# Kernel tuning notes

Measured on AMD Instinct MI355X. Metric: run time of the kernel, lower is better.

## Reference

```python
import math
import jax, jax.numpy as jnp
import numpy as np

D_MODEL = 1024
NUM_HEADS = 16
D_K = D_MODEL // NUM_HEADS
THETA = 10000.0
MAX_SEQ_LEN = 2048
BATCH = 2
SEQ = 2048


def build_rope_matrices(theta, d_k, max_seq_len):
    # Faithful to the torch buffer: per-position d_k x d_k tridiagonal rotation matrix.
    k = jnp.arange(d_k)
    inv_freq = jnp.power(theta, -2.0 * (k // 2) / d_k)  # [d_k]
    pos = jnp.arange(max_seq_len, dtype=jnp.float32)[:, None]  # [S,1]
    ang = pos * inv_freq[None, :]  # [S, d_k]
    cos_v = jnp.cos(ang)  # main diagonal
    sin_v = jnp.sin(jnp.where(k % 2 == 0, ang, 0.0))[:, :-1]  # sub/super diagonal, len d_k-1

    def mk(c, s):
        return jnp.diag(c) + jnp.diag(s, -1) + jnp.diag(-s, 1)

    return jax.vmap(mk)(cos_v, sin_v)  # [max_seq_len, d_k, d_k]


def setup_inputs() -> dict:
    key = jax.random.key(0)
    k1, k2, k3 = jax.random.split(key, 3)
    x = jax.random.normal(k1, (BATCH, SEQ, D_MODEL), dtype=jnp.float32)
    token_positions = jnp.arange(SEQ, dtype=jnp.int64 if jax.config.jax_enable_x64 else jnp.int32)
    # trunc_normal init approximated by scaled normal (same distribution family / scale)
    std_attn = 2.0 / (D_MODEL + 3 * D_MODEL)
    std_out = 2.0 / (D_MODEL + D_MODEL)
    W_attn = jax.random.normal(k2, (3 * NUM_HEADS * D_K, D_MODEL), dtype=jnp.float32) * std_attn
    W_out = jax.random.normal(k3, (D_MODEL, NUM_HEADS * D_K), dtype=jnp.float32) * std_out
    rope = build_rope_matrices(THETA, D_K, MAX_SEQ_LEN)
    return {"x": x, "W_attn": W_attn, "W_out": W_out, "rope": rope,
            "token_positions": token_positions}


def reference(x, W_attn, W_out, rope, token_positions):
    B, S, _ = x.shape
    # QKV projection: '... d_in, d_out d_in -> ... d_out'
    proj = jnp.einsum('bsd,ed->bse', x, W_attn)  # [B,S,3*H*dk]
    proj = proj.reshape(B, S, 3, NUM_HEADS, D_K)
    proj = jnp.transpose(proj, (2, 0, 3, 1, 4))  # [3,B,H,S,dk]
    Q, K, V = proj[0], proj[1], proj[2]
    # RoPE via per-position matrix multiply (faithful to module)
    R = rope[token_positions]  # [S, dk, dk]
    Q = jnp.einsum('sij,bhsj->bhsi', R, Q)
    K = jnp.einsum('sij,bhsj->bhsi', R, K)
    # naive causal attention with full score matrix (faithful)
    scores = jnp.einsum('bhnd,bhmd->bhnm', Q, K) / math.sqrt(D_K)
    causal = jnp.tril(jnp.ones((S, S), dtype=bool))
    scores = jnp.where(causal, scores, -jnp.inf)
    attn = jax.nn.softmax(scores, axis=-1)
    attended = jnp.einsum('bhnm,bhmd->bhnd', attn, V)  # [B,H,S,dk]
    concat = jnp.transpose(attended, (0, 2, 1, 3)).reshape(B, S, NUM_HEADS * D_K)
    return jnp.einsum('bse,de->bsd', concat, W_out)
```

## Files before the change

### kernel.cpp

```cpp
#include <hip/hip_runtime.h>
#include <math.h>

#define B_SZ 2
#define SEQ 2048
#define DMODEL 1024
#define NH 16
#define DK 64
#define NQKV 3072
#define M_ROWS 4096

#define NEG_BIG (-3.0e38f)
#define SCL 0.18033688011112042f

typedef short short8 __attribute__((ext_vector_type(8)));
typedef float v4f __attribute__((ext_vector_type(4)));
typedef unsigned short ushort_t;

__device__ inline ushort_t f2bf(float f) {
    unsigned u = __float_as_uint(f);
    u += 0x7fffu + ((u >> 16) & 1u);
    return (ushort_t)(u >> 16);
}

__device__ __forceinline__ unsigned cvt_pk_bf16(float lo, float hi) {
    unsigned r;
    asm("v_cvt_pk_bf16_f32 %0, %1, %2" : "=v"(r) : "v"(lo), "v"(hi));
    return r;
}
__device__ __forceinline__ void permlane32_swap(unsigned &a, unsigned &b) {
    asm("v_permlane32_swap_b32 %0, %1" : "+v"(a), "+v"(b));
}
__device__ __forceinline__ void permlane16_swap(unsigned &a, unsigned &b) {
    asm("v_permlane16_swap_b32 %0, %1" : "+v"(a), "+v"(b));
}

__device__ __forceinline__ void gl_lds16(const ushort_t* g, ushort_t* l) {
    __builtin_amdgcn_global_load_lds(
        (const __attribute__((address_space(1))) unsigned int*)g,
        (__attribute__((address_space(3))) unsigned int*)l, 16, 0, 0);
}

__global__ __launch_bounds__(256) void prep_kernel(
    const float* __restrict__ x, const float* __restrict__ Wa,
    const float* __restrict__ Wo, const float* __restrict__ rope,
    ushort_t* __restrict__ xb, ushort_t* __restrict__ Wab, ushort_t* __restrict__ Wob,
    float* __restrict__ cosT, float* __restrict__ sinT)
{
    const int bid = blockIdx.x;
    if (bid < 8192) {
        const float* src; ushort_t* dst; int i;
        if (bid < 4096)      { src = x;  dst = xb;  i = bid * 256 + threadIdx.x; }
        else if (bid < 7168) { src = Wa; dst = Wab; i = (bid - 4096) * 256 + threadIdx.x; }
        else                 { src = Wo; dst = Wob; i = (bid - 7168) * 256 + threadIdx.x; }
        float4 v = reinterpret_cast<const float4*>(src)[i];
        ushort4 r;
        r.x = f2bf(v.x); r.y = f2bf(v.y); r.z = f2bf(v.z); r.w = f2bf(v.w);
        reinterpret_cast<ushort4*>(dst)[i] = r;
    } else {
        const int i = (bid - 8192) * 256 + threadIdx.x;
        const int p = i >> 6, d = i & 63;
        const float* Rp = rope + (size_t)p * 4096;
        const float c = Rp[d * 64 + d];
        const float s = Rp[(d | 1) * 64 + (d & ~1)];
        cosT[i] = c;
        sinT[i] = (d & 1) ? s : -s;
    }
}

#define ES_STRIDE 136
extern __shared__ ushort_t qkv_smem[];

__global__ __launch_bounds__(256) void qkv_mfma_kernel(
    const ushort_t* __restrict__ xb,
    const ushort_t* __restrict__ Wab,
    const float* __restrict__ cosT, const float* __restrict__ sinT,
    const int* __restrict__ tpos,
    ushort_t* __restrict__ Qb, ushort_t* __restrict__ Kb, ushort_t* __restrict__ Vtb)
{
    ushort_t* Es = qkv_smem;

    const int tid = threadIdx.x;
    const int w = tid >> 6, lane = tid & 63;
    const int lm = lane & 15, g = lane >> 4;
    const int wm = (w >> 1) * 64, wn = (w & 1) * 64;
    const int e0 = blockIdx.x * 128, m0 = blockIdx.y * 128;

    int srow[8], skc[8];
#pragma unroll
    for (int j = 0; j < 8; ++j) {
        const int c = tid + 256 * j;
        const int cm = c & 1023;
        const int row = cm >> 3, pp = cm & 7;
        srow[j] = row;
        skc[j] = (pp ^ (row & 7)) * 8;
    }

    v4f acc[4][4] = {};

    for (int k0 = 0; k0 < DMODEL; k0 += 64) {
        __syncthreads();
#pragma unroll
        for (int j = 0; j < 4; ++j)
            gl_lds16(&Wab[(size_t)(e0 + srow[j]) * DMODEL + k0 + skc[j]],
                     &qkv_smem[(tid + 256 * j) * 8]);
#pragma unroll
        for (int j = 4; j < 8; ++j)
            gl_lds16(&xb [(size_t)(m0 + srow[j]) * DMODEL + k0 + skc[j]],
                     &qkv_smem[(tid + 256 * j) * 8]);
        __syncthreads();

#pragma unroll
        for (int kb = 0; kb < 2; ++kb) {
            short8 af[4], bfr[4];
#pragma unroll
            for (int mf = 0; mf < 4; ++mf) {
                const int r = wm + mf * 16 + lm;
                af[mf] = *reinterpret_cast<const short8*>(
                    &qkv_smem[(r * 8 + ((kb * 4 + g) ^ (r & 7))) * 8]);
            }
#pragma unroll
            for (int nf = 0; nf < 4; ++nf) {
                const int r = wn + nf * 16 + lm;
                bfr[nf] = *reinterpret_cast<const short8*>(
                    &qkv_smem[8192 + (r * 8 + ((kb * 4 + g) ^ (r & 7))) * 8]);
            }
#pragma unroll
            for (int mf = 0; mf < 4; ++mf)
#pragma unroll
                for (int nf = 0; nf < 4; ++nf)
                    acc[mf][nf] = __builtin_amdgcn_mfma_f32_16x16x32_bf16(af[mf], bfr[nf], acc[mf][nf], 0, 0, 0);
        }
    }

    __syncthreads();

    const int which = e0 >> 10;
    const int h0 = (e0 & 1023) >> 6;
    const int bb = m0 >> 11, s0 = m0 & 2047;

    if (which < 2) {
        ushort_t* buf = (which == 0) ? Qb : Kb;
        const float qs = (which == 0) ? SCL : 1.0f;
#pragma unroll
        for (int mf = 0; mf < 4; ++mf) {
            const int ebase = wm + mf * 16 + g * 4;
            const int d0 = (e0 + ebase) & 63;
#pragma unroll
            for (int nf = 0; nf < 4; ++nf) {
                const int sloc = wn + nf * 16 + lm;
                float v[4] = {acc[mf][nf][0], acc[mf][nf][1], acc[mf][nf][2], acc[mf][nf][3]};
                const int p = tpos[s0 + sloc];
                const float4 c4 = *reinterpret_cast<const float4*>(&cosT[p * 64 + d0]);
                const float4 s4 = *reinterpret_cast<const float4*>(&sinT[p * 64 + d0]);
                const float r0 = (c4.x * v[0] + s4.x * v[1]) * qs;
                const float r1 = (c4.y * v[1] + s4.y * v[0]) * qs;
                const float r2 = (c4.z * v[2] + s4.z * v[3]) * qs;
                const float r3 = (c4.w * v[3] + s4.w * v[2]) * qs;
                uint2 pp;
                pp.x = (unsigned)f2bf(r0) | ((unsigned)f2bf(r1) << 16);
                pp.y = (unsigned)f2bf(r2) | ((unsigned)f2bf(r3) << 16);
                *reinterpret_cast<uint2*>(&Es[sloc * ES_STRIDE + ebase]) = pp;
            }
        }
        __syncthreads();
#pragma unroll
        for (int hh = 0; hh < 2; ++hh) {
            ushort_t* dst = buf + (((size_t)bb * NH + h0 + hh) * SEQ + s0) * DK;
#pragma unroll
            for (int t = 0; t < 4; ++t) {
                const int o = (t * 256 + tid) * 8;
                const int sloc = o >> 6, d = o & 63;
                const short8 vv = *reinterpret_cast<const short8*>(&Es[sloc * ES_STRIDE + hh * 64 + d]);
                *reinterpret_cast<short8*>(&dst[o]) = vv;
            }
        }
    } else {
#pragma unroll
        for (int mf = 0; mf < 4; ++mf) {
            const int ebase = wm + mf * 16 + g * 4;
#pragma unroll
            for (int nf = 0; nf < 4; ++nf) {
                const int sloc = wn + nf * 16 + lm;
                Es[(ebase + 0) * ES_STRIDE + sloc] = f2bf(acc[mf][nf][0]);
                Es[(ebase + 1) * ES_STRIDE + sloc] = f2bf(acc[mf][nf][1]);
                Es[(ebase + 2) * ES_STRIDE + sloc] = f2bf(acc[mf][nf][2]);
                Es[(ebase + 3) * ES_STRIDE + sloc] = f2bf(acc[mf][nf][3]);
            }
        }
        __syncthreads();
#pragma unroll
        for (int t = 0; t < 8; ++t) {
            const int c = t * 256 + tid;
            const int hh = c >> 10, cm = c & 1023;
            const int d = cm >> 4, s8c = (cm & 15) * 8;
            const short8 vv = *reinterpret_cast<const short8*>(&Es[(hh * 64 + d) * ES_STRIDE + s8c]);
            ushort_t* dst = Vtb + ((size_t)bb * NH + h0 + hh) * SEQ * DK + (size_t)d * SEQ + s0 + s8c;
            *reinterpret_cast<short8*>(dst) = vv;
        }
    }
}

#define ATTN_STEP(QF0, QF1, QROW, LACC, OACC, DIAG, C0)                           \
    {                                                                             \
        v4f sacc[4] = {};                                                         \
        _Pragma("unroll")                                                         \
        for (int nf = 0; nf < 4; ++nf) {                                          \
            sacc[nf] = __builtin_amdgcn_mfma_f32_16x16x32_bf16(kf[nf][0], QF0, sacc[nf], 0, 0, 0); \
            sacc[nf] = __builtin_amdgcn_mfma_f32_16x16x32_bf16(kf[nf][1], QF1, sacc[nf], 0, 0, 0); \
        }                                                                         \
        if (DIAG) {                                                               \
            _Pragma("unroll")                                                     \
            for (int nf = 0; nf < 4; ++nf)                                        \
                _Pragma("unroll")                                                 \
                for (int reg = 0; reg < 4; ++reg) {                               \
                    const int kv = (C0) + nf * 16 + g * 4 + reg;                  \
                    if (kv > (QROW)) sacc[nf][reg] = NEG_BIG;                     \
                }                                                                 \
        }                                                                         \
        unsigned pk0[8];                                                          \
        _Pragma("unroll")                                                         \
        for (int nf = 0; nf < 4; ++nf) {                                          \
            pk0[nf * 2]     = cvt_pk_bf16(exp2f(sacc[nf][0]), exp2f(sacc[nf][1])); \
            pk0[nf * 2 + 1] = cvt_pk_bf16(exp2f(sacc[nf][2]), exp2f(sacc[nf][3])); \
        }                                                                         \
        _Pragma("unroll")                                                         \
        for (int kc = 0; kc < 2; ++kc) {                                          \
            unsigned x0 = pk0[kc * 4 + 0], y0 = pk0[kc * 4 + 2];                  \
            unsigned x1 = pk0[kc * 4 + 1], y1 = pk0[kc * 4 + 3];                  \
            permlane32_swap(x0, y0); permlane16_swap(x0, y0);                     \
            permlane32_swap(x1, y1); permlane16_swap(x1, y1);                     \
            union { unsigned u[4]; short8 s; } pu;                                \
            pu.u[0] = x0; pu.u[1] = x1; pu.u[2] = y0; pu.u[3] = y1;               \
            const short8 pf = pu.s;                                               \
            LACC = __builtin_amdgcn_mfma_f32_16x16x32_bf16(ones8, pf, LACC, 0, 0, 0); \
            _Pragma("unroll")                                                     \
            for (int df = 0; df < 4; ++df)                                        \
                OACC[df] = __builtin_amdgcn_mfma_f32_16x16x32_bf16(vf[df][kc], pf, OACC[df], 0, 0, 0); \
        }                                                                         \
    }

__global__ __launch_bounds__(256, 2) void attn_mfma_kernel(
    const ushort_t* __restrict__ Qb, const ushort_t* __restrict__ Kb,
    const ushort_t* __restrict__ Vtb, ushort_t* __restrict__ attb)
{
    __shared__ ushort_t Ks[2][64][72];
    __shared__ ushort_t Vs[2][64][72];

    const int tid = threadIdx.x;
    const int w = tid >> 6, lane = tid & 63;
    const int lm = lane & 15, g = lane >> 4, lk8 = g * 8;

    const int u = blockIdx.x;
    const int h = blockIdx.y, b = blockIdx.z;
    const size_t ho = ((size_t)b * NH + h) * SEQ * DK;
    const ushort_t* Qh = Qb + ho;
    const ushort_t* Kh = Kb + ho;
    const ushort_t* Vth = Vtb + ho;

    const int rr0 = tid >> 3, cc80 = (tid & 7) * 8;
    const int rr1 = (tid + 256) >> 3, cc81 = ((tid + 256) & 7) * 8;

    const int it1 = u, it2 = 31 - u;
    const int qrowA = it1 * 64 + w * 16 + lm;
    const int qrowB = it2 * 64 + w * 16 + lm;

    const short8 qa0 = *reinterpret_cast<const short8*>(&Qh[(size_t)qrowA * DK + lk8]);
    const short8 qa1 = *reinterpret_cast<const short8*>(&Qh[(size_t)qrowA * DK + 32 + lk8]);
    const short8 qb0 = *reinterpret_cast<const short8*>(&Qh[(size_t)qrowB * DK + lk8]);
    const short8 qb1 = *reinterpret_cast<const short8*>(&Qh[(size_t)qrowB * DK + 32 + lk8]);

    const short8 ones8 = {16256, 16256, 16256, 16256, 16256, 16256, 16256, 16256};

    v4f laccA = {}, laccB = {};
    v4f OA[4] = {}, OB[4] = {};

    short8 kreg[2], vreg[2];
    kreg[0] = *reinterpret_cast<const short8*>(&Kh[(size_t)rr0 * DK + cc80]);
    kreg[1] = *reinterpret_cast<const short8*>(&Kh[(size_t)rr1 * DK + cc81]);
    vreg[0] = *reinterpret_cast<const short8*>(&Vth[(size_t)rr0 * SEQ + cc80]);
    vreg[1] = *reinterpret_cast<const short8*>(&Vth[(size_t)rr1 * SEQ + cc81]);

    for (int jt = 0; jt <= it2; ++jt) {
        const int c0 = jt * 64;
        const int bufi = jt & 1;
        ushort_t (*Ksb)[72] = Ks[bufi];
        ushort_t (*Vsb)[72] = Vs[bufi];

        *reinterpret_cast<short8*>(&Ksb[rr0][cc80]) = kreg[0];
        *reinterpret_cast<short8*>(&Ksb[rr1][cc81]) = kreg[1];
        *reinterpret_cast<short8*>(&Vsb[rr0][cc80]) = vreg[0];
        *reinterpret_cast<short8*>(&Vsb[rr1][cc81]) = vreg[1];

        if (jt < it2) {
            const int c0n = c0 + 64;
            kreg[0] = *reinterpret_cast<const short8*>(&Kh[(size_t)(c0n + rr0) * DK + cc80]);
            kreg[1] = *reinterpret_cast<const short8*>(&Kh[(size_t)(c0n + rr1) * DK + cc81]);
            vreg[0] = *reinterpret_cast<const short8*>(&Vth[(size_t)rr0 * SEQ + c0n + cc80]);
            vreg[1] = *reinterpret_cast<const short8*>(&Vth[(size_t)rr1 * SEQ + c0n + cc81]);
        }

        __syncthreads();

        short8 kf[4][2], vf[4][2];
#pragma unroll
        for (int nf = 0; nf < 4; ++nf) {
            kf[nf][0] = *reinterpret_cast<const short8*>(&Ksb[nf * 16 + lm][lk8]);
            kf[nf][1] = *reinterpret_cast<const short8*>(&Ksb[nf * 16 + lm][32 + lk8]);
        }
#pragma unroll
        for (int df = 0; df < 4; ++df) {
            vf[df][0] = *reinterpret_cast<const short8*>(&Vsb[df * 16 + lm][lk8]);
            vf[df][1] = *reinterpret_cast<const short8*>(&Vsb[df * 16 + lm][32 + lk8]);
        }

        ATTN_STEP(qb0, qb1, qrowB, laccB, OB, (jt == it2), c0)
        if (jt <= it1) {
            ATTN_STEP(qa0, qa1, qrowA, laccA, OA, (jt == it1), c0)
        }
    }

    {
        const float inv = 1.0f / laccA[0];
#pragma unroll
        for (int df = 0; df < 4; ++df) {
            uint2 st;
            st.x = cvt_pk_bf16(OA[df][0] * inv, OA[df][1] * inv);
            st.y = cvt_pk_bf16(OA[df][2] * inv, OA[df][3] * inv);
            *reinterpret_cast<uint2*>(
                &attb[((size_t)b * SEQ + qrowA) * DMODEL + h * DK + df * 16 + g * 4]) = st;
        }
    }
    {
        const float inv = 1.0f / laccB[0];
#pragma unroll
        for (int df = 0; df < 4; ++df) {
            uint2 st;
            st.x = cvt_pk_bf16(OB[df][0] * inv, OB[df][1] * inv);
            st.y = cvt_pk_bf16(OB[df][2] * inv, OB[df][3] * inv);
            *reinterpret_cast<uint2*>(
                &attb[((size_t)b * SEQ + qrowB) * DMODEL + h * DK + df * 16 + g * 4]) = st;
        }
    }
}

__global__ __launch_bounds__(256) void out_mfma_kernel(
    const ushort_t* __restrict__ attb,
    const ushort_t* __restrict__ Wob,
    float* __restrict__ out)
{
    __shared__ ushort_t smem[16384];

    const int tid = threadIdx.x;
    const int w = tid >> 6, lane = tid & 63;
    const int lm = lane & 15, g = lane >> 4;
    const int wm = (w >> 1) * 64, wn = (w & 1) * 64;
    const int m0 = blockIdx.y * 128, n0 = blockIdx.x * 128;

    int srow[8], skc[8];
#pragma unroll
    for (int j = 0; j < 8; ++j) {
        const int c = tid + 256 * j;
        const int cm = c & 1023;
        const int row = cm >> 3, pp = cm & 7;
        srow[j] = row;
        skc[j] = (pp ^ (row & 7)) * 8;
    }

    v4f acc[4][4] = {};

    for (int k0 = 0; k0 < DMODEL; k0 += 64) {
        __syncthreads();
#pragma unroll
        for (int j = 0; j < 4; ++j)
            gl_lds16(&attb[(size_t)(m0 + srow[j]) * DMODEL + k0 + skc[j]],
                     &smem[(tid + 256 * j) * 8]);
#pragma unroll
        for (int j = 4; j < 8; ++j)
            gl_lds16(&Wob[(size_t)(n0 + srow[j]) * DMODEL + k0 + skc[j]],
                     &smem[(tid + 256 * j) * 8]);
        __syncthreads();

#pragma unroll
        for (int kb = 0; kb < 2; ++kb) {
            short8 af[4], bfr[4];
#pragma unroll
            for (int mf = 0; mf < 4; ++mf) {
                const int r = wm + mf * 16 + lm;
                af[mf] = *reinterpret_cast<const short8*>(
                    &smem[(r * 8 + ((kb * 4 + g) ^ (r & 7))) * 8]);
            }
#pragma unroll
            for (int nf = 0; nf < 4; ++nf) {
                const int r = wn + nf * 16 + lm;
                bfr[nf] = *reinterpret_cast<const short8*>(
                    &smem[8192 + (r * 8 + ((kb * 4 + g) ^ (r & 7))) * 8]);
            }
#pragma unroll
            for (int mf = 0; mf < 4; ++mf)
#pragma unroll
                for (int nf = 0; nf < 4; ++nf)
                    acc[mf][nf] = __builtin_amdgcn_mfma_f32_16x16x32_bf16(af[mf], bfr[nf], acc[mf][nf], 0, 0, 0);
        }
    }

#pragma unroll
    for (int mf = 0; mf < 4; ++mf)
#pragma unroll
        for (int reg = 0; reg < 4; ++reg) {
            const int m = m0 + wm + mf * 16 + g * 4 + reg;
#pragma unroll
            for (int nf = 0; nf < 4; ++nf) {
                const int n = n0 + wn + nf * 16 + lm;
                out[(size_t)m * DMODEL + n] = acc[mf][nf][reg];
            }
        }
}

extern "C" void kernel_launch(void* const* d_in, const int* in_sizes, int n_in,
                              void* d_out, int out_size, void* d_ws, size_t ws_size,
                              hipStream_t stream) {
    (void)in_sizes; (void)n_in; (void)out_size; (void)ws_size;

    const float* x    = (const float*)d_in[0];
    const float* Wa   = (const float*)d_in[1];
    const float* Wo   = (const float*)d_in[2];
    const float* rope = (const float*)d_in[3];
    const int*   tp   = (const int*)d_in[4];
    float* out = (float*)d_out;

    char* ws = (char*)d_ws;
    ushort_t* xb   = (ushort_t*)(ws);
    ushort_t* Wab  = (ushort_t*)(ws + (8u << 20));
    ushort_t* Wob  = (ushort_t*)(ws + (14u << 20));
    float*    cosT = (float*)   (ws + (16u << 20));
    float*    sinT = (float*)   (ws + (16u << 20) + (512u << 10));
    ushort_t* Qb   = (ushort_t*)(ws + (17u << 20));
    ushort_t* Kb   = (ushort_t*)(ws + (25u << 20));
    ushort_t* Vtb  = (ushort_t*)(ws + (33u << 20));
    ushort_t* attb = (ushort_t*)(ws + (41u << 20));

    dim3 blk(256);
    prep_kernel<<<dim3(8704), blk, 0, stream>>>(x, Wa, Wo, rope, xb, Wab, Wob, cosT, sinT);

    const size_t qkv_lds = 128 * ES_STRIDE * sizeof(ushort_t);
    qkv_mfma_kernel<<<dim3(NQKV / 128, M_ROWS / 128), blk, qkv_lds, stream>>>(
        xb, Wab, cosT, sinT, tp, Qb, Kb, Vtb);
    attn_mfma_kernel<<<dim3(16, NH, B_SZ), blk, 0, stream>>>(Qb, Kb, Vtb, attb);
    out_mfma_kernel<<<dim3(DMODEL / 128, M_ROWS / 128), blk, 0, stream>>>(attb, Wob, out);
}
```

Baseline: 217.4 us.

## Double-buffer LDS tiles and swizzle block order in QKV and output GEMMs

Both projection GEMMs now use two LDS buffers so the next K-tile's global-to-LDS loads are issued before computing the current tile, with explicit vmcnt waits and barriers replacing the two syncthreads per iteration. Block indices are remapped with an XCD-style swizzle so neighbouring tiles share L2, and MFMA sections get raised wave priority. The cost is double the LDS (64KB per block), which may reduce occupancy, and hand-placed waitcnt that depends on the exact count of outstanding loads.

```diff
diff --git a/kernel.cpp b/kernel.cpp
--- a/kernel.cpp
+++ b/kernel.cpp
@@ -68,7 +68,16 @@
 }
 
 #define ES_STRIDE 136
-extern __shared__ ushort_t qkv_smem[];
+
+#define QKV_STAGE(bofs, k0s)                                                   \
+    _Pragma("unroll")                                                          \
+    for (int j = 0; j < 4; ++j)                                                \
+        gl_lds16(&Wab[(size_t)(e0 + srow[j]) * DMODEL + (k0s) + skc[j]],       \
+                 &qkv_smem[(bofs) + (tid + 256 * j) * 8]);                     \
+    _Pragma("unroll")                                                          \
+    for (int j = 4; j < 8; ++j)                                                \
+        gl_lds16(&xb[(size_t)(m0 + srow[j]) * DMODEL + (k0s) + skc[j]],        \
+                 &qkv_smem[(bofs) + (tid + 256 * j) * 8]);
 
 __global__ __launch_bounds__(256) void qkv_mfma_kernel(
     const ushort_t* __restrict__ xb,
@@ -77,13 +86,17 @@
     const int* __restrict__ tpos,
     ushort_t* __restrict__ Qb, ushort_t* __restrict__ Kb, ushort_t* __restrict__ Vtb)
 {
+    __shared__ ushort_t qkv_smem[32768];
     ushort_t* Es = qkv_smem;
 
     const int tid = threadIdx.x;
     const int w = tid >> 6, lane = tid & 63;
     const int lm = lane & 15, g = lane >> 4;
     const int wm = (w >> 1) * 64, wn = (w & 1) * 64;
-    const int e0 = blockIdx.x * 128, m0 = blockIdx.y * 128;
+
+    const int lid = blockIdx.y * 24 + blockIdx.x;
+    const int swz = (lid & 7) * 96 + (lid >> 3);
+    const int e0 = (swz % 24) * 128, m0 = (swz / 24) * 128;
 
     int srow[8], skc[8];
 #pragma unroll
@@ -97,18 +110,23 @@
 
     v4f acc[4][4] = {};
 
-    for (int k0 = 0; k0 < DMODEL; k0 += 64) {
-        __syncthreads();
-#pragma unroll
-        for (int j = 0; j < 4; ++j)
-            gl_lds16(&Wab[(size_t)(e0 + srow[j]) * DMODEL + k0 + skc[j]],
-                     &qkv_smem[(tid + 256 * j) * 8]);
-#pragma unroll
-        for (int j = 4; j < 8; ++j)
-            gl_lds16(&xb [(size_t)(m0 + srow[j]) * DMODEL + k0 + skc[j]],
-                     &qkv_smem[(tid + 256 * j) * 8]);
-        __syncthreads();
-
+    QKV_STAGE(0, 0);
+
+    for (int t = 0; t < 16; ++t) {
+        const int bofs = (t & 1) << 14;
+        if (t < 15) {
+            const int nofs = ((t + 1) & 1) << 14;
+            QKV_STAGE(nofs, (t + 1) * 64);
+            __builtin_amdgcn_sched_barrier(0);
+            asm volatile("s_waitcnt vmcnt(8)" ::: "memory");
+        } else {
+            __builtin_amdgcn_sched_barrier(0);
+            asm volatile("s_waitcnt vmcnt(0)" ::: "memory");
+        }
+        __builtin_amdgcn_s_barrier();
+        __builtin_amdgcn_sched_barrier(0);
+
+        __builtin_amdgcn_s_setprio(1);
 #pragma unroll
         for (int kb = 0; kb < 2; ++kb) {
             short8 af[4], bfr[4];
@@ -116,13 +134,13 @@
             for (int mf = 0; mf < 4; ++mf) {
                 const int r = wm + mf * 16 + lm;
                 af[mf] = *reinterpret_cast<const short8*>(
-                    &qkv_smem[(r * 8 + ((kb * 4 + g) ^ (r & 7))) * 8]);
+                    &qkv_smem[bofs + (r * 8 + ((kb * 4 + g) ^ (r & 7))) * 8]);
             }
 #pragma unroll
             for (int nf = 0; nf < 4; ++nf) {
                 const int r = wn + nf * 16 + lm;
                 bfr[nf] = *reinterpret_cast<const short8*>(
-                    &qkv_smem[8192 + (r * 8 + ((kb * 4 + g) ^ (r & 7))) * 8]);
+                    &qkv_smem[bofs + 8192 + (r * 8 + ((kb * 4 + g) ^ (r & 7))) * 8]);
             }
 #pragma unroll
             for (int mf = 0; mf < 4; ++mf)
@@ -130,6 +148,11 @@
                 for (int nf = 0; nf < 4; ++nf)
                     acc[mf][nf] = __builtin_amdgcn_mfma_f32_16x16x32_bf16(af[mf], bfr[nf], acc[mf][nf], 0, 0, 0);
         }
+        __builtin_amdgcn_s_setprio(0);
+
+        __builtin_amdgcn_sched_barrier(0);
+        __builtin_amdgcn_s_barrier();
+        __builtin_amdgcn_sched_barrier(0);
     }
 
     __syncthreads();
@@ -343,18 +366,31 @@
     }
 }
 
+#define OUT_STAGE(bofs, k0s)                                                   \
+    _Pragma("unroll")                                                          \
+    for (int j = 0; j < 4; ++j)                                                \
+        gl_lds16(&attb[(size_t)(m0 + srow[j]) * DMODEL + (k0s) + skc[j]],      \
+                 &smem[(bofs) + (tid + 256 * j) * 8]);                         \
+    _Pragma("unroll")                                                          \
+    for (int j = 4; j < 8; ++j)                                                \
+        gl_lds16(&Wob[(size_t)(n0 + srow[j]) * DMODEL + (k0s) + skc[j]],       \
+                 &smem[(bofs) + (tid + 256 * j) * 8]);
+
 __global__ __launch_bounds__(256) void out_mfma_kernel(
     const ushort_t* __restrict__ attb,
     const ushort_t* __restrict__ Wob,
     float* __restrict__ out)
 {
-    __shared__ ushort_t smem[16384];
+    __shared__ ushort_t smem[32768];
 
     const int tid = threadIdx.x;
     const int w = tid >> 6, lane = tid & 63;
     const int lm = lane & 15, g = lane >> 4;
     const int wm = (w >> 1) * 64, wn = (w & 1) * 64;
-    const int m0 = blockIdx.y * 128, n0 = blockIdx.x * 128;
+
+    const int lid = blockIdx.y * 8 + blockIdx.x;
+    const int swz = (lid & 7) * 32 + (lid >> 3);
+    const int m0 = (swz >> 3) * 128, n0 = (swz & 7) * 128;
 
     int srow[8], skc[8];
 #pragma unroll
@@ -368,18 +404,23 @@
 
     v4f acc[4][4] = {};
 
-    for (int k0 = 0; k0 < DMODEL; k0 += 64) {
-        __syncthreads();
-#pragma unroll
-        for (int j = 0; j < 4; ++j)
-            gl_lds16(&attb[(size_t)(m0 + srow[j]) * DMODEL + k0 + skc[j]],
-                     &smem[(tid + 256 * j) * 8]);
-#pragma unroll
-        for (int j = 4; j < 8; ++j)
-            gl_lds16(&Wob[(size_t)(n0 + srow[j]) * DMODEL + k0 + skc[j]],
-                     &smem[(tid + 256 * j) * 8]);
-        __syncthreads();
-
+    OUT_STAGE(0, 0);
+
+    for (int t = 0; t < 16; ++t) {
+        const int bofs = (t & 1) << 14;
+        if (t < 15) {
+            const int nofs = ((t + 1) & 1) << 14;
+            OUT_STAGE(nofs, (t + 1) * 64);
+            __builtin_amdgcn_sched_barrier(0);
+            asm volatile("s_waitcnt vmcnt(8)" ::: "memory");
+        } else {
+            __builtin_amdgcn_sched_barrier(0);
+            asm volatile("s_waitcnt vmcnt(0)" ::: "memory");
+        }
+        __builtin_amdgcn_s_barrier();
+        __builtin_amdgcn_sched_barrier(0);
+
+        __builtin_amdgcn_s_setprio(1);
 #pragma unroll
         for (int kb = 0; kb < 2; ++kb) {
             short8 af[4], bfr[4];
@@ -387,13 +428,13 @@
             for (int mf = 0; mf < 4; ++mf) {
                 const int r = wm + mf * 16 + lm;
                 af[mf] = *reinterpret_cast<const short8*>(
-                    &smem[(r * 8 + ((kb * 4 + g) ^ (r & 7))) * 8]);
+                    &smem[bofs + (r * 8 + ((kb * 4 + g) ^ (r & 7))) * 8]);
             }
 #pragma unroll
             for (int nf = 0; nf < 4; ++nf) {
                 const int r = wn + nf * 16 + lm;
                 bfr[nf] = *reinterpret_cast<const short8*>(
-                    &smem[8192 + (r * 8 + ((kb * 4 + g) ^ (r & 7))) * 8]);
+                    &smem[bofs + 8192 + (r * 8 + ((kb * 4 + g) ^ (r & 7))) * 8]);
             }
 #pragma unroll
             for (int mf = 0; mf < 4; ++mf)
@@ -401,6 +442,11 @@
                 for (int nf = 0; nf < 4; ++nf)
                     acc[mf][nf] = __builtin_amdgcn_mfma_f32_16x16x32_bf16(af[mf], bfr[nf], acc[mf][nf], 0, 0, 0);
         }
+        __builtin_amdgcn_s_setprio(0);
+
+        __builtin_amdgcn_sched_barrier(0);
+        __builtin_amdgcn_s_barrier();
+        __builtin_amdgcn_sched_barrier(0);
     }
 
 #pragma unroll
@@ -442,8 +488,7 @@
     dim3 blk(256);
     prep_kernel<<<dim3(8704), blk, 0, stream>>>(x, Wa, Wo, rope, xb, Wab, Wob, cosT, sinT);
 
-    const size_t qkv_lds = 128 * ES_STRIDE * sizeof(ushort_t);
-    qkv_mfma_kernel<<<dim3(NQKV / 128, M_ROWS / 128), blk, qkv_lds, stream>>>(
+    qkv_mfma_kernel<<<dim3(NQKV / 128, M_ROWS / 128), blk, 0, stream>>>(
         xb, Wab, cosT, sinT, tp, Qb, Kb, Vtb);
     attn_mfma_kernel<<<dim3(16, NH, B_SZ), blk, 0, stream>>>(Qb, Kb, Vtb, attb);
     out_mfma_kernel<<<dim3(DMODEL / 128, M_ROWS / 128), blk, 0, stream>>>(attb, Wob, out);
```

After: 207.8 us. 1.05x faster.
